# Optimization experiments

Measured on AMD Instinct MI355X. Metric: run time of the kernel, lower is better.

The kernel has to match this reference:

```python
import jax, jax.numpy as jnp
import numpy as np

B, T, E, H = 8, 2048, 1024, 1024
_LN_EPS = 1e-3  # keras LayerNormalization default epsilon


def _ln(x, g, b):
    mu = jnp.mean(x, axis=-1, keepdims=True)
    var = jnp.var(x, axis=-1, keepdims=True)
    return (x - mu) * jax.lax.rsqrt(var + _LN_EPS) * g + b


def _time_shift(x):
    # ZeroPadding1D((1,0)) applied to x[:, :-1]: shift right by one, zero at t=0
    return jnp.pad(x[:, :-1], ((0, 0), (1, 0), (0, 0)))


def _wkv(k, v, w, u):
    """RWKV-v4 wkv: numerically stabilized exponential-decay recurrence.
    k, v: (B, T, H); w = -exp(time_decay) (negative), u = time_first: (H,).
    wkv_t = (sum_{i<t} e^{(t-1-i)w + k_i} v_i + e^{u + k_t} v_t)
          / (sum_{i<t} e^{(t-1-i)w + k_i}     + e^{u + k_t})
    """
    Bk, Tk, Hk = k.shape

    def step(carry, kv_t):
        aa, bb, pp = carry  # running num/den with shared log-scale pp
        kt, vt = kv_t
        ww = u + kt
        q = jnp.maximum(pp, ww)
        e1 = jnp.exp(pp - q)
        e2 = jnp.exp(ww - q)
        out = (e1 * aa + e2 * vt) / (e1 * bb + e2)
        ww2 = pp + w
        q2 = jnp.maximum(ww2, kt)
        e1b = jnp.exp(ww2 - q2)
        e2b = jnp.exp(kt - q2)
        return (e1b * aa + e2b * vt, e1b * bb + e2b, q2), out

    init = (jnp.zeros((Bk, Hk), k.dtype),
            jnp.zeros((Bk, Hk), k.dtype),
            jnp.full((Bk, Hk), -1e38, k.dtype))
    kT = jnp.swapaxes(k, 0, 1)  # (T, B, H)
    vT = jnp.swapaxes(v, 0, 1)
    _, outs = jax.lax.scan(step, init, (kT, vT))
    return jnp.swapaxes(outs, 0, 1)


def setup_inputs() -> dict:
    key = jax.random.key(0)
    ks = jax.random.split(key, 20)

    def glorot(k, shape):
        lim = np.sqrt(6.0 / (shape[0] + shape[1]))
        return jax.random.uniform(k, shape, jnp.float32, -lim, lim)

    return {
        'inputs': jax.random.normal(ks[0], (B, T, E), jnp.float32),
        'ln1_g': jnp.ones((E,), jnp.float32),
        'ln1_b': jnp.zeros((E,), jnp.float32),
        'ln2_g': jnp.ones((E,), jnp.float32),
        'ln2_b': jnp.zeros((E,), jnp.float32),
        'tm_mix_k': jax.random.uniform(ks[1], (E,), jnp.float32, 0.0, 2.0 / E),
        'tm_mix_v': jax.random.uniform(ks[2], (E,), jnp.float32, 0.0, 2.0 / E),
        'tm_mix_r': jax.random.uniform(ks[3], (E,), jnp.float32, 0.0, (2.0 / E) ** 0.5),
        'tm_Wk': glorot(ks[4], (E, H)),
        'tm_Wv': glorot(ks[5], (E, H)),
        'tm_Wr': glorot(ks[6], (E, H)),
        'time_decay': jax.random.uniform(ks[7], (H,), jnp.float32, 0.0, 0.5),
        'time_first': jax.random.uniform(ks[8], (H,), jnp.float32, 0.0, 0.05),
        'Wo': glorot(ks[9], (H, E)),
        'cm_mix_k': jax.random.uniform(ks[10], (E,), jnp.float32, 0.0, 2.0 / E),
        'cm_mix_r': jax.random.uniform(ks[11], (E,), jnp.float32, 0.0, 2.0 / E),
        'cm_Wk': glorot(ks[12], (E, 4 * H)),
        'cm_Wv': glorot(ks[13], (4 * H, E)),
        'cm_Wr': glorot(ks[14], (E, E)),
    }


def reference(inputs, ln1_g, ln1_b, ln2_g, ln2_b,
              tm_mix_k, tm_mix_v, tm_mix_r, tm_Wk, tm_Wv, tm_Wr,
              time_decay, time_first, Wo,
              cm_mix_k, cm_mix_r, cm_Wk, cm_Wv, cm_Wr):
    x = inputs

    # ---- time mixing ----
    h = _ln(x, ln1_g, ln1_b)
    h1 = _time_shift(h)
    xk = h * tm_mix_k + h1 * (1.0 - tm_mix_k)
    xv = h * tm_mix_v + h1 * (1.0 - tm_mix_v)
    xr = h * tm_mix_r + h1 * (1.0 - tm_mix_r)
    k = xk @ tm_Wk
    v = xv @ tm_Wv
    r = xr @ tm_Wr
    wkv = _wkv(k, v, -jnp.exp(time_decay), time_first)
    x = x + (jax.nn.sigmoid(r) * wkv) @ Wo

    # ---- channel mixing ----
    h = _ln(x, ln2_g, ln2_b)
    h1 = _time_shift(h)
    xk = h * cm_mix_k + h1 * (1.0 - cm_mix_k)
    xr = h * cm_mix_r + h1 * (1.0 - cm_mix_r)
    kc = jnp.square(jax.nn.relu(xk @ cm_Wk))  # (B, T, 4H)
    rc = jax.nn.sigmoid(xr @ cm_Wr)
    x = x + rc * (kc @ cm_Wv)
    return x
```

## Files before the change

### kernel.cpp

```cpp
#include <hip/hip_runtime.h>
#include <stdint.h>
#include <stddef.h>

#define Bb 8
#define Tt 2048
#define Ee 1024
#define Hh 1024
#define ROWS (Bb * Tt)
#define CC 32
#define LL 64

typedef __attribute__((ext_vector_type(8))) _Float16 half8v;
typedef __attribute__((ext_vector_type(4))) _Float16 half4v;
typedef __attribute__((ext_vector_type(4))) float f32x4;

#define GL2LDS(gp, lp)                                                        \
  __builtin_amdgcn_global_load_lds(                                          \
      (const __attribute__((address_space(1))) void*)(gp),                   \
      (__attribute__((address_space(3))) void*)(lp), 16, 0, 0)

__global__ __launch_bounds__(256)
void wtrans_kernel(const float* __restrict__ W, _Float16* __restrict__ Wt,
                   const int K, const int N) {
  __shared__ float tle[64][65];
  const int ntn = N >> 6;
  const int tn = blockIdx.x % ntn;
  const int tk = blockIdx.x / ntn;
  const int tid = threadIdx.x;
  const int r = tid >> 4;
  const int c4 = (tid & 15) * 4;
#pragma unroll
  for (int i = 0; i < 4; i++) {
    const int row = r + i * 16;
    const float4 v = *reinterpret_cast<const float4*>(
        &W[(size_t)(tk * 64 + row) * N + tn * 64 + c4]);
    tle[row][c4] = v.x; tle[row][c4 + 1] = v.y;
    tle[row][c4 + 2] = v.z; tle[row][c4 + 3] = v.w;
  }
  __syncthreads();
#pragma unroll
  for (int j = 0; j < 2; j++) {
    const int ch = tid + j * 256;
    const int n = ch >> 3;
    const int k8 = (ch & 7) * 8;
    half8v o;
#pragma unroll
    for (int m = 0; m < 8; m++) o[m] = (_Float16)tle[k8 + m][n];
    *reinterpret_cast<half8v*>(&Wt[(size_t)(tn * 64 + n) * K + tk * 64 + k8]) = o;
  }
}

__global__ __launch_bounds__(256)
void ln_kernel(const float* __restrict__ x, const float* __restrict__ gw,
               const float* __restrict__ bw, _Float16* __restrict__ h) {
  const int row = blockIdx.x * 4 + (threadIdx.x >> 6);
  const int lane = threadIdx.x & 63;
  const float4* xr = reinterpret_cast<const float4*>(x + (size_t)row * Ee);
  float4 v[4];
  float s = 0.f, sq = 0.f;
#pragma unroll
  for (int i = 0; i < 4; i++) {
    v[i] = xr[lane + i * 64];
    s += v[i].x + v[i].y + v[i].z + v[i].w;
    sq += v[i].x * v[i].x + v[i].y * v[i].y + v[i].z * v[i].z + v[i].w * v[i].w;
  }
#pragma unroll
  for (int o = 32; o > 0; o >>= 1) {
    s += __shfl_xor(s, o);
    sq += __shfl_xor(sq, o);
  }
  const float mu = s * (1.f / Ee);
  const float var = sq * (1.f / Ee) - mu * mu;
  const float rs = rsqrtf(var + 1e-3f);
  const float4* gr = reinterpret_cast<const float4*>(gw);
  const float4* br = reinterpret_cast<const float4*>(bw);
#pragma unroll
  for (int i = 0; i < 4; i++) {
    const int c = lane + i * 64;
    const float4 g4 = gr[c], b4 = br[c];
    half4v o;
    o[0] = (_Float16)((v[i].x - mu) * rs * g4.x + b4.x);
    o[1] = (_Float16)((v[i].y - mu) * rs * g4.y + b4.y);
    o[2] = (_Float16)((v[i].z - mu) * rs * g4.z + b4.z);
    o[3] = (_Float16)((v[i].w - mu) * rs * g4.w + b4.w);
    *reinterpret_cast<half4v*>(&h[(size_t)row * Ee + (size_t)c * 4]) = o;
  }
}

template <bool HASV>
__global__ __launch_bounds__(256)
void mix_kernel(const _Float16* __restrict__ h, const float* __restrict__ mk,
                const float* __restrict__ mv, const float* __restrict__ mr,
                _Float16* __restrict__ xk, _Float16* __restrict__ xv,
                _Float16* __restrict__ xr) {
  const int gid = blockIdx.x * 256 + threadIdx.x;
  const int row = gid >> 8;
  const int c = gid & 255;
  const int t = row & (Tt - 1);
  const size_t o = (size_t)row * 1024 + (size_t)c * 4;
  const half4v hv4 = *reinterpret_cast<const half4v*>(&h[o]);
  float hx[4] = {(float)hv4[0], (float)hv4[1], (float)hv4[2], (float)hv4[3]};
  float h1[4] = {0.f, 0.f, 0.f, 0.f};
  if (t > 0) {
    const half4v p4 = *reinterpret_cast<const half4v*>(&h[o - 1024]);
    h1[0] = (float)p4[0]; h1[1] = (float)p4[1];
    h1[2] = (float)p4[2]; h1[3] = (float)p4[3];
  }
  const float4 k4 = reinterpret_cast<const float4*>(mk)[c];
  const float4 r4 = reinterpret_cast<const float4*>(mr)[c];
  const float km[4] = {k4.x, k4.y, k4.z, k4.w};
  const float rm[4] = {r4.x, r4.y, r4.z, r4.w};
  half4v ok, orr;
#pragma unroll
  for (int j = 0; j < 4; j++) {
    ok[j] = (_Float16)(hx[j] * km[j] + h1[j] * (1.f - km[j]));
    orr[j] = (_Float16)(hx[j] * rm[j] + h1[j] * (1.f - rm[j]));
  }
  *reinterpret_cast<half4v*>(&xk[o]) = ok;
  *reinterpret_cast<half4v*>(&xr[o]) = orr;
  if constexpr (HASV) {
    const float4 v4 = reinterpret_cast<const float4*>(mv)[c];
    const float vm[4] = {v4.x, v4.y, v4.z, v4.w};
    half4v ov;
#pragma unroll
    for (int j = 0; j < 4; j++)
      ov[j] = (_Float16)(hx[j] * vm[j] + h1[j] * (1.f - vm[j]));
    *reinterpret_cast<half4v*>(&xv[o]) = ov;
  }
}

__global__ __launch_bounds__(256)
void wkv_pass1(const _Float16* __restrict__ kb, const _Float16* __restrict__ vb,
               const float* __restrict__ decay,
               float* __restrict__ aal, float* __restrict__ bbl,
               float* __restrict__ ppl) {
  const int gid = blockIdx.x * 256 + threadIdx.x;
  const int h = gid & 1023;
  const int rest = gid >> 10;
  const int c = rest & (CC - 1);
  const int b = rest >> 5;
  const float w = -__expf(decay[h]);
  const size_t base = ((size_t)b * Tt + (size_t)c * LL) * Hh + h;
  float aa = 0.f, bb = 0.f, pp = -1e38f;
  for (int i0 = 0; i0 < LL; i0 += 8) {
    float kt[8], vt[8];
#pragma unroll
    for (int j = 0; j < 8; j++) {
      const size_t idx = base + (size_t)(i0 + j) * Hh;
      kt[j] = (float)kb[idx];
      vt[j] = (float)vb[idx];
    }
#pragma unroll
    for (int j = 0; j < 8; j++) {
      const float ww2 = pp + w;
      const float q2 = fmaxf(ww2, kt[j]);
      const float e1 = __expf(ww2 - q2);
      const float e2 = __expf(kt[j] - q2);
      aa = e1 * aa + e2 * vt[j];
      bb = e1 * bb + e2;
      pp = q2;
    }
  }
  const int sidx = (b * CC + c) * Hh + h;
  aal[sidx] = aa; bbl[sidx] = bb; ppl[sidx] = pp;
}

__global__ __launch_bounds__(256)
void wkv_pass2(const float* __restrict__ decay,
               const float* __restrict__ aal, const float* __restrict__ bbl,
               const float* __restrict__ ppl,
               float* __restrict__ aap, float* __restrict__ bbp,
               float* __restrict__ ppp) {
  const int gid = blockIdx.x * 256 + threadIdx.x;
  const int h = gid & 1023;
  const int b = gid >> 10;
  const float w = -__expf(decay[h]);
  const float Lw = (float)LL * w;
  float aa = 0.f, bb = 0.f, pp = -1e38f;
#pragma unroll
  for (int c = 0; c < CC; c++) {
    const int sidx = (b * CC + c) * Hh + h;
    aap[sidx] = aa; bbp[sidx] = bb; ppp[sidx] = pp;
    const float la = aal[sidx], lb = bbl[sidx], lp = ppl[sidx];
    const float sp = pp + Lw;
    const float q = fmaxf(sp, lp);
    const float e1 = __expf(sp - q);
    const float e2 = __expf(lp - q);
    aa = e1 * aa + e2 * la;
    bb = e1 * bb + e2 * lb;
    pp = q;
  }
}

__global__ __launch_bounds__(256)
void wkv_pass3(const _Float16* __restrict__ kb, const _Float16* __restrict__ vb,
               const _Float16* __restrict__ rb,
               const float* __restrict__ decay, const float* __restrict__ first,
               const float* __restrict__ aap, const float* __restrict__ bbp,
               const float* __restrict__ ppp, _Float16* __restrict__ ab) {
  const int gid = blockIdx.x * 256 + threadIdx.x;
  const int h = gid & 1023;
  const int rest = gid >> 10;
  const int c = rest & (CC - 1);
  const int b = rest >> 5;
  const float w = -__expf(decay[h]);
  const float u = first[h];
  const int sidx = (b * CC + c) * Hh + h;
  float aa = aap[sidx], bb = bbp[sidx], pp = ppp[sidx];
  const size_t base = ((size_t)b * Tt + (size_t)c * LL) * Hh + h;
  for (int i0 = 0; i0 < LL; i0 += 8) {
    float kt[8], vt[8], rr[8];
#pragma unroll
    for (int j = 0; j < 8; j++) {
      const size_t idx = base + (size_t)(i0 + j) * Hh;
      kt[j] = (float)kb[idx];
      vt[j] = (float)vb[idx];
      rr[j] = (float)rb[idx];
    }
#pragma unroll
    for (int j = 0; j < 8; j++) {
      const float ww = u + kt[j];
      const float q = fmaxf(pp, ww);
      const float e1 = __expf(pp - q);
      const float e2 = __expf(ww - q);
      const float out = (e1 * aa + e2 * vt[j]) / (e1 * bb + e2);
      const float sr = 1.f / (1.f + __expf(-rr[j]));
      ab[base + (size_t)(i0 + j) * Hh] = (_Float16)(sr * out);
      const float ww2 = pp + w;
      const float q2 = fmaxf(ww2, kt[j]);
      const float e1b = __expf(ww2 - q2);
      const float e2b = __expf(kt[j] - q2);
      aa = e1b * aa + e2b * vt[j];
      bb = e1b * bb + e2b;
      pp = q2;
    }
  }
}

template <int EPI>
__global__ __launch_bounds__(256)
void gemm97(const _Float16* __restrict__ A, const int ldA,
            const _Float16* __restrict__ Bt, const int ldB,
            const int N, const int K, const int nbx,
            float* __restrict__ outF, _Float16* __restrict__ outH,
            const float* __restrict__ res, const _Float16* __restrict__ scale) {
  alignas(16) __shared__ _Float16 As[128 * 64];
  alignas(16) __shared__ _Float16 Bs[128 * 64];
  const int tid = threadIdx.x;
  const int lane = tid & 63;
  const int w = tid >> 6;
  const int wm = w >> 1, wn = w & 1;
  const int r0 = lane & 15, kg = lane >> 4;
  const int cpx = gridDim.x >> 3;
  const int wg = ((int)blockIdx.x & 7) * cpx + ((int)blockIdx.x >> 3);
  const int bm = (wg / nbx) * 128;
  const int bn = (wg % nbx) * 128;
  const int NT = K >> 6;

  const int srow = lane >> 3;
  const int sslot = lane & 7;
  f32x4 acc[4][4];
#pragma unroll
  for (int i = 0; i < 4; i++)
#pragma unroll
    for (int j = 0; j < 4; j++) acc[i][j] = (f32x4){0.f, 0.f, 0.f, 0.f};

  for (int t = 0; t < NT; ++t) {
#pragma unroll
    for (int i = 0; i < 4; i++) {
      const int chunk = i * 4 + w;
      const int row = chunk * 8 + srow;
      const int gsl = sslot ^ (row & 7);
      GL2LDS(A + (size_t)(bm + row) * ldA + (size_t)t * 64 + gsl * 8,
             &As[chunk * 512]);
    }
#pragma unroll
    for (int i = 0; i < 4; i++) {
      const int chunk = i * 4 + w;
      const int row = chunk * 8 + srow;
      const int gsl = sslot ^ (row & 7);
      GL2LDS(Bt + (size_t)(bn + row) * ldB + (size_t)t * 64 + gsl * 8,
             &Bs[chunk * 512]);
    }
    __syncthreads();
    half8v af[4][2], bf[4][2];
#pragma unroll
    for (int m = 0; m < 4; m++)
#pragma unroll
      for (int kk = 0; kk < 2; kk++) {
        const int row = wm * 64 + m * 16 + r0;
        const int c = kk * 4 + kg;
        af[m][kk] = *reinterpret_cast<const half8v*>(
            &As[row * 64 + ((c ^ (row & 7)) << 3)]);
      }
#pragma unroll
    for (int n = 0; n < 4; n++)
#pragma unroll
      for (int kk = 0; kk < 2; kk++) {
        const int row = wn * 64 + n * 16 + r0;
        const int c = kk * 4 + kg;
        bf[n][kk] = *reinterpret_cast<const half8v*>(
            &Bs[row * 64 + ((c ^ (row & 7)) << 3)]);
      }
#pragma unroll
    for (int m = 0; m < 4; m++)
#pragma unroll
      for (int n = 0; n < 4; n++)
#pragma unroll
        for (int kk = 0; kk < 2; kk++)
          acc[m][n] = __builtin_amdgcn_mfma_f32_16x16x32_f16(
              af[m][kk], bf[n][kk], acc[m][n], 0, 0, 0);
    __syncthreads();
  }

#pragma unroll
  for (int m = 0; m < 4; m++) {
#pragma unroll
    for (int n = 0; n < 4; n++) {
#pragma unroll
      for (int i = 0; i < 4; i++) {
        const int row = bm + wm * 64 + m * 16 + kg * 4 + i;
        const int col = bn + wn * 64 + n * 16 + r0;
        const size_t idx = (size_t)row * N + col;
        const float val = acc[m][n][i];
        if constexpr (EPI == 0) {
          outH[idx] = (_Float16)val;
        } else if constexpr (EPI == 1) {
          const float tt = fmaxf(val, 0.f);
          outH[idx] = (_Float16)(tt * tt);
        } else if constexpr (EPI == 2) {
          outH[idx] = (_Float16)(1.f / (1.f + __expf(-val)));
        } else if constexpr (EPI == 3) {
          outF[idx] = res[idx] + val;
        } else {
          outF[idx] = outF[idx] + (float)scale[idx] * val;
        }
      }
    }
  }
}

extern "C" void kernel_launch(void* const* d_in, const int* in_sizes, int n_in,
                              void* d_out, int out_size, void* d_ws,
                              size_t ws_size, hipStream_t stream) {
  (void)in_sizes; (void)n_in; (void)out_size; (void)ws_size;
  const float* x_in      = (const float*)d_in[0];
  const float* ln1_g     = (const float*)d_in[1];
  const float* ln1_b     = (const float*)d_in[2];
  const float* ln2_g     = (const float*)d_in[3];
  const float* ln2_b     = (const float*)d_in[4];
  const float* tm_mix_k  = (const float*)d_in[5];
  const float* tm_mix_v  = (const float*)d_in[6];
  const float* tm_mix_r  = (const float*)d_in[7];
  const float* tm_Wk     = (const float*)d_in[8];
  const float* tm_Wv     = (const float*)d_in[9];
  const float* tm_Wr     = (const float*)d_in[10];
  const float* time_decay= (const float*)d_in[11];
  const float* time_first= (const float*)d_in[12];
  const float* Wo        = (const float*)d_in[13];
  const float* cm_mix_k  = (const float*)d_in[14];
  const float* cm_mix_r  = (const float*)d_in[15];
  const float* cm_Wk     = (const float*)d_in[16];
  const float* cm_Wv     = (const float*)d_in[17];
  const float* cm_Wr     = (const float*)d_in[18];
  float* out = (float*)d_out;
  char* ws = (char*)d_ws;
  const size_t MB = 1024ull * 1024ull;

  _Float16* WkT   = (_Float16*)(ws + 0 * MB);
  _Float16* WvT   = (_Float16*)(ws + 2 * MB);
  _Float16* WrT   = (_Float16*)(ws + 4 * MB);
  _Float16* WoT   = (_Float16*)(ws + 6 * MB);
  _Float16* cmWkT = (_Float16*)(ws + 8 * MB);
  _Float16* cmWvT = (_Float16*)(ws + 16 * MB);
  _Float16* cmWrT = (_Float16*)(ws + 24 * MB);
  float* aal = (float*)(ws + 0 * MB);
  float* bbl = (float*)(ws + 1 * MB);
  float* ppl = (float*)(ws + 2 * MB);
  float* aap = (float*)(ws + 3 * MB);
  float* bbp = (float*)(ws + 4 * MB);
  float* ppp = (float*)(ws + 5 * MB);
  _Float16* h16   = (_Float16*)(ws + 26 * MB);
  _Float16* xk    = (_Float16*)(ws + 58 * MB);
  _Float16* xv    = (_Float16*)(ws + 90 * MB);
  _Float16* xr    = (_Float16*)(ws + 122 * MB);
  _Float16* kb    = h16;
  _Float16* vb    = xk;
  _Float16* rb    = xv;
  _Float16* ab    = xr;
  _Float16* h2    = (_Float16*)(ws + 26 * MB);
  _Float16* xr2   = (_Float16*)(ws + 58 * MB);
  _Float16* xk2   = (_Float16*)(ws + 90 * MB);
  _Float16* rc    = (_Float16*)(ws + 122 * MB);
  _Float16* kc    = (_Float16*)(ws + 26 * MB);

  wtrans_kernel<<<dim3(256), 256, 0, stream>>>(tm_Wk, WkT, 1024, 1024);
  wtrans_kernel<<<dim3(256), 256, 0, stream>>>(tm_Wv, WvT, 1024, 1024);
  wtrans_kernel<<<dim3(256), 256, 0, stream>>>(tm_Wr, WrT, 1024, 1024);
  wtrans_kernel<<<dim3(256), 256, 0, stream>>>(Wo, WoT, 1024, 1024);
  wtrans_kernel<<<dim3(1024), 256, 0, stream>>>(cm_Wk, cmWkT, 1024, 4096);
  wtrans_kernel<<<dim3(1024), 256, 0, stream>>>(cm_Wv, cmWvT, 4096, 1024);
  wtrans_kernel<<<dim3(256), 256, 0, stream>>>(cm_Wr, cmWrT, 1024, 1024);

  ln_kernel<<<dim3(ROWS / 4), 256, 0, stream>>>(x_in, ln1_g, ln1_b, h16);
  mix_kernel<true><<<dim3(ROWS), 256, 0, stream>>>(h16, tm_mix_k, tm_mix_v,
                                                   tm_mix_r, xk, xv, xr);
  gemm97<0><<<dim3(128 * 8), 256, 0, stream>>>(xk, 1024, WkT, 1024, 1024, 1024,
                                               8, nullptr, kb, nullptr, nullptr);
  gemm97<0><<<dim3(128 * 8), 256, 0, stream>>>(xv, 1024, WvT, 1024, 1024, 1024,
                                               8, nullptr, vb, nullptr, nullptr);
  gemm97<0><<<dim3(128 * 8), 256, 0, stream>>>(xr, 1024, WrT, 1024, 1024, 1024,
                                               8, nullptr, rb, nullptr, nullptr);
  wkv_pass1<<<dim3(Bb * CC * Hh / 256), 256, 0, stream>>>(kb, vb, time_decay,
                                                          aal, bbl, ppl);
  wkv_pass2<<<dim3(Bb * Hh / 256), 256, 0, stream>>>(time_decay, aal, bbl, ppl,
                                                     aap, bbp, ppp);
  wkv_pass3<<<dim3(Bb * CC * Hh / 256), 256, 0, stream>>>(
      kb, vb, rb, time_decay, time_first, aap, bbp, ppp, ab);
  gemm97<3><<<dim3(128 * 8), 256, 0, stream>>>(ab, 1024, WoT, 1024, 1024, 1024,
                                               8, out, nullptr, x_in, nullptr);

  ln_kernel<<<dim3(ROWS / 4), 256, 0, stream>>>(out, ln2_g, ln2_b, h2);
  mix_kernel<false><<<dim3(ROWS), 256, 0, stream>>>(h2, cm_mix_k, nullptr,
                                                    cm_mix_r, xk2, nullptr, xr2);
  gemm97<2><<<dim3(128 * 8), 256, 0, stream>>>(xr2, 1024, cmWrT, 1024, 1024,
                                               1024, 8, nullptr, rc, nullptr,
                                               nullptr);
  for (int half = 0; half < 2; half++) {
    const _Float16* Bk = cmWkT + (size_t)half * 2048 * 1024;
    const _Float16* Bv = cmWvT + (size_t)half * 2048;
    gemm97<1><<<dim3(128 * 16), 256, 0, stream>>>(xk2, 1024, Bk, 1024, 2048,
                                                  1024, 16, nullptr, kc, nullptr,
                                                  nullptr);
    gemm97<4><<<dim3(128 * 8), 256, 0, stream>>>(kc, 2048, Bv, 4096, 1024,
                                                 2048, 8, out, nullptr, nullptr,
                                                 rc);
  }
}
```

Baseline: 864.0 us.

## Replace GEMM with 256x256-tile double-buffered kernel loading B directly to registers

The 128x128 GEMM with 256 threads becomes a 256x256-tile kernel with 512 threads (8 waves, 2x4). Only A is staged into double-buffered dynamic LDS; B fragments are loaded straight from global memory into registers, prefetched one K-step ahead. Explicit vmcnt waits, a single barrier per iteration and s_setprio around the MFMA block are meant to overlap loads with compute and cut LDS traffic and sync cost. The trade-offs are heavy register pressure from 128 accumulators plus two B fragment sets, uncoalesced direct B loads, and far fewer workgroups (256 for most GEMMs) to fill the GPU.

```diff
diff --git a/kernel.cpp b/kernel.cpp
--- a/kernel.cpp
+++ b/kernel.cpp
@@ -18,6 +18,10 @@
   __builtin_amdgcn_global_load_lds(                                          \
       (const __attribute__((address_space(1))) void*)(gp),                   \
       (__attribute__((address_space(3))) void*)(lp), 16, 0, 0)
+
+#define VMCNT(n) __builtin_amdgcn_s_waitcnt(0xF70 | (n))
+#define BAR __builtin_amdgcn_s_barrier()
+#define SCHED0 __builtin_amdgcn_sched_barrier(0)
 
 __global__ __launch_bounds__(256)
 void wtrans_kernel(const float* __restrict__ W, _Float16* __restrict__ Wt,
@@ -238,91 +242,104 @@
 }
 
 template <int EPI>
-__global__ __launch_bounds__(256)
-void gemm97(const _Float16* __restrict__ A, const int ldA,
+__global__ __launch_bounds__(512)
+void gemmBD(const _Float16* __restrict__ A, const int ldA,
             const _Float16* __restrict__ Bt, const int ldB,
             const int N, const int K, const int nbx,
             float* __restrict__ outF, _Float16* __restrict__ outH,
             const float* __restrict__ res, const _Float16* __restrict__ scale) {
-  alignas(16) __shared__ _Float16 As[128 * 64];
-  alignas(16) __shared__ _Float16 Bs[128 * 64];
+  extern __shared__ _Float16 sA[];
   const int tid = threadIdx.x;
   const int lane = tid & 63;
   const int w = tid >> 6;
-  const int wm = w >> 1, wn = w & 1;
+  const int wm = w >> 2, wn = w & 3;
   const int r0 = lane & 15, kg = lane >> 4;
   const int cpx = gridDim.x >> 3;
   const int wg = ((int)blockIdx.x & 7) * cpx + ((int)blockIdx.x >> 3);
-  const int bm = (wg / nbx) * 128;
-  const int bn = (wg % nbx) * 128;
+  const int bm = (wg / nbx) * 256;
+  const int bn = (wg % nbx) * 256;
   const int NT = K >> 6;
 
-  const int srow = lane >> 3;
-  const int sslot = lane & 7;
-  f32x4 acc[4][4];
-#pragma unroll
-  for (int i = 0; i < 4; i++)
+  f32x4 acc[8][4];
+#pragma unroll
+  for (int i = 0; i < 8; i++)
 #pragma unroll
     for (int j = 0; j < 4; j++) acc[i][j] = (f32x4){0.f, 0.f, 0.f, 0.f};
 
+  auto stageA = [&](int t, int p) {
+#pragma unroll
+    for (int i = 0; i < 4; i++) {
+      const int chunk = w * 4 + i;
+      const int row = chunk * 8 + (lane >> 3);
+      const int gs = (lane & 7) ^ (row & 7);
+      GL2LDS(A + (size_t)(bm + row) * ldA + (size_t)t * 64 + gs * 8,
+             sA + p * 16384 + chunk * 512);
+    }
+  };
+  auto loadB = [&](int t, half8v (&b)[4][2]) {
+#pragma unroll
+    for (int fc = 0; fc < 4; fc++)
+#pragma unroll
+      for (int kk = 0; kk < 2; kk++)
+        b[fc][kk] = *reinterpret_cast<const half8v*>(
+            Bt + (size_t)(bn + wn * 64 + fc * 16 + r0) * ldB +
+            (size_t)t * 64 + (size_t)(kk * 4 + kg) * 8);
+  };
+
+  half8v bC[4][2], bN[4][2];
+
+  stageA(0, 0);
+  VMCNT(0);
+  loadB(0, bC);
+  BAR;
+
   for (int t = 0; t < NT; ++t) {
-#pragma unroll
-    for (int i = 0; i < 4; i++) {
-      const int chunk = i * 4 + w;
-      const int row = chunk * 8 + srow;
-      const int gsl = sslot ^ (row & 7);
-      GL2LDS(A + (size_t)(bm + row) * ldA + (size_t)t * 64 + gsl * 8,
-             &As[chunk * 512]);
-    }
-#pragma unroll
-    for (int i = 0; i < 4; i++) {
-      const int chunk = i * 4 + w;
-      const int row = chunk * 8 + srow;
-      const int gsl = sslot ^ (row & 7);
-      GL2LDS(Bt + (size_t)(bn + row) * ldB + (size_t)t * 64 + gsl * 8,
-             &Bs[chunk * 512]);
-    }
-    __syncthreads();
-    half8v af[4][2], bf[4][2];
-#pragma unroll
-    for (int m = 0; m < 4; m++)
+    const int p = t & 1;
+    if (t + 1 < NT) stageA(t + 1, p ^ 1);
+    SCHED0;
+    half8v af[8][2];
+#pragma unroll
+    for (int fr = 0; fr < 8; fr++)
 #pragma unroll
       for (int kk = 0; kk < 2; kk++) {
-        const int row = wm * 64 + m * 16 + r0;
-        const int c = kk * 4 + kg;
-        af[m][kk] = *reinterpret_cast<const half8v*>(
-            &As[row * 64 + ((c ^ (row & 7)) << 3)]);
+        const int row = wm * 128 + fr * 16 + r0;
+        af[fr][kk] = *reinterpret_cast<const half8v*>(
+            sA + p * 16384 + row * 64 + (((kk * 4 + kg) ^ (row & 7)) << 3));
       }
-#pragma unroll
-    for (int n = 0; n < 4; n++)
-#pragma unroll
-      for (int kk = 0; kk < 2; kk++) {
-        const int row = wn * 64 + n * 16 + r0;
-        const int c = kk * 4 + kg;
-        bf[n][kk] = *reinterpret_cast<const half8v*>(
-            &Bs[row * 64 + ((c ^ (row & 7)) << 3)]);
-      }
-#pragma unroll
-    for (int m = 0; m < 4; m++)
-#pragma unroll
-      for (int n = 0; n < 4; n++)
+    __builtin_amdgcn_s_setprio(1);
+#pragma unroll
+    for (int fr = 0; fr < 8; fr++)
+#pragma unroll
+      for (int fc = 0; fc < 4; fc++)
 #pragma unroll
         for (int kk = 0; kk < 2; kk++)
-          acc[m][n] = __builtin_amdgcn_mfma_f32_16x16x32_f16(
-              af[m][kk], bf[n][kk], acc[m][n], 0, 0, 0);
-    __syncthreads();
-  }
-
-#pragma unroll
-  for (int m = 0; m < 4; m++) {
-#pragma unroll
-    for (int n = 0; n < 4; n++) {
+          acc[fr][fc] = __builtin_amdgcn_mfma_f32_16x16x32_f16(
+              af[fr][kk], bC[fc][kk], acc[fr][fc], 0, 0, 0);
+    __builtin_amdgcn_s_setprio(0);
+    SCHED0;
+    if (t + 1 < NT) {
+      loadB(t + 1, bN);
+      VMCNT(8);
+    } else {
+      VMCNT(0);
+    }
+    BAR;
+#pragma unroll
+    for (int fc = 0; fc < 4; fc++)
+#pragma unroll
+      for (int kk = 0; kk < 2; kk++) bC[fc][kk] = bN[fc][kk];
+  }
+
+#pragma unroll
+  for (int fr = 0; fr < 8; fr++) {
+#pragma unroll
+    for (int fc = 0; fc < 4; fc++) {
 #pragma unroll
       for (int i = 0; i < 4; i++) {
-        const int row = bm + wm * 64 + m * 16 + kg * 4 + i;
-        const int col = bn + wn * 64 + n * 16 + r0;
+        const int row = bm + wm * 128 + fr * 16 + (lane >> 4) * 4 + i;
+        const int col = bn + wn * 64 + fc * 16 + r0;
         const size_t idx = (size_t)row * N + col;
-        const float val = acc[m][n][i];
+        const float val = acc[fr][fc][i];
         if constexpr (EPI == 0) {
           outH[idx] = (_Float16)val;
         } else if constexpr (EPI == 1) {
@@ -394,6 +411,17 @@
   _Float16* rc    = (_Float16*)(ws + 122 * MB);
   _Float16* kc    = (_Float16*)(ws + 26 * MB);
 
+  const int SMEM = 65536;
+  static bool attr_done = false;
+  if (!attr_done) {
+    hipFuncSetAttribute((const void*)gemmBD<0>, hipFuncAttributeMaxDynamicSharedMemorySize, SMEM);
+    hipFuncSetAttribute((const void*)gemmBD<1>, hipFuncAttributeMaxDynamicSharedMemorySize, SMEM);
+    hipFuncSetAttribute((const void*)gemmBD<2>, hipFuncAttributeMaxDynamicSharedMemorySize, SMEM);
+    hipFuncSetAttribute((const void*)gemmBD<3>, hipFuncAttributeMaxDynamicSharedMemorySize, SMEM);
+    hipFuncSetAttribute((const void*)gemmBD<4>, hipFuncAttributeMaxDynamicSharedMemorySize, SMEM);
+    attr_done = true;
+  }
+
   wtrans_kernel<<<dim3(256), 256, 0, stream>>>(tm_Wk, WkT, 1024, 1024);
   wtrans_kernel<<<dim3(256), 256, 0, stream>>>(tm_Wv, WvT, 1024, 1024);
   wtrans_kernel<<<dim3(256), 256, 0, stream>>>(tm_Wr, WrT, 1024, 1024);
@@ -405,35 +433,39 @@
   ln_kernel<<<dim3(ROWS / 4), 256, 0, stream>>>(x_in, ln1_g, ln1_b, h16);
   mix_kernel<true><<<dim3(ROWS), 256, 0, stream>>>(h16, tm_mix_k, tm_mix_v,
                                                    tm_mix_r, xk, xv, xr);
-  gemm97<0><<<dim3(128 * 8), 256, 0, stream>>>(xk, 1024, WkT, 1024, 1024, 1024,
-                                               8, nullptr, kb, nullptr, nullptr);
-  gemm97<0><<<dim3(128 * 8), 256, 0, stream>>>(xv, 1024, WvT, 1024, 1024, 1024,
-                                               8, nullptr, vb, nullptr, nullptr);
-  gemm97<0><<<dim3(128 * 8), 256, 0, stream>>>(xr, 1024, WrT, 1024, 1024, 1024,
-                                               8, nullptr, rb, nullptr, nullptr);
+  gemmBD<0><<<dim3(64 * 4), 512, SMEM, stream>>>(xk, 1024, WkT, 1024, 1024,
+                                                 1024, 4, nullptr, kb, nullptr,
+                                                 nullptr);
+  gemmBD<0><<<dim3(64 * 4), 512, SMEM, stream>>>(xv, 1024, WvT, 1024, 1024,
+                                                 1024, 4, nullptr, vb, nullptr,
+                                                 nullptr);
+  gemmBD<0><<<dim3(64 * 4), 512, SMEM, stream>>>(xr, 1024, WrT, 1024, 1024,
+                                                 1024, 4, nullptr, rb, nullptr,
+                                                 nullptr);
   wkv_pass1<<<dim3(Bb * CC * Hh / 256), 256, 0, stream>>>(kb, vb, time_decay,
                                                           aal, bbl, ppl);
   wkv_pass2<<<dim3(Bb * Hh / 256), 256, 0, stream>>>(time_decay, aal, bbl, ppl,
                                                      aap, bbp, ppp);
   wkv_pass3<<<dim3(Bb * CC * Hh / 256), 256, 0, stream>>>(
       kb, vb, rb, time_decay, time_first, aap, bbp, ppp, ab);
-  gemm97<3><<<dim3(128 * 8), 256, 0, stream>>>(ab, 1024, WoT, 1024, 1024, 1024,
-                                               8, out, nullptr, x_in, nullptr);
+  gemmBD<3><<<dim3(64 * 4), 512, SMEM, stream>>>(ab, 1024, WoT, 1024, 1024,
+                                                 1024, 4, out, nullptr, x_in,
+                                                 nullptr);
 
   ln_kernel<<<dim3(ROWS / 4), 256, 0, stream>>>(out, ln2_g, ln2_b, h2);
   mix_kernel<false><<<dim3(ROWS), 256, 0, stream>>>(h2, cm_mix_k, nullptr,
                                                     cm_mix_r, xk2, nullptr, xr2);
-  gemm97<2><<<dim3(128 * 8), 256, 0, stream>>>(xr2, 1024, cmWrT, 1024, 1024,
-                                               1024, 8, nullptr, rc, nullptr,
-                                               nullptr);
+  gemmBD<2><<<dim3(64 * 4), 512, SMEM, stream>>>(xr2, 1024, cmWrT, 1024, 1024,
+                                                 1024, 4, nullptr, rc, nullptr,
+                                                 nullptr);
   for (int half = 0; half < 2; half++) {
     const _Float16* Bk = cmWkT + (size_t)half * 2048 * 1024;
     const _Float16* Bv = cmWvT + (size_t)half * 2048;
-    gemm97<1><<<dim3(128 * 16), 256, 0, stream>>>(xk2, 1024, Bk, 1024, 2048,
-                                                  1024, 16, nullptr, kc, nullptr,
-                                                  nullptr);
-    gemm97<4><<<dim3(128 * 8), 256, 0, stream>>>(kc, 2048, Bv, 4096, 1024,
-                                                 2048, 8, out, nullptr, nullptr,
-                                                 rc);
-  }
-}
+    gemmBD<1><<<dim3(64 * 8), 512, SMEM, stream>>>(xk2, 1024, Bk, 1024, 2048,
+                                                   1024, 8, nullptr, kc,
+                                                   nullptr, nullptr);
+    gemmBD<4><<<dim3(64 * 4), 512, SMEM, stream>>>(kc, 2048, Bv, 4096, 1024,
+                                                   2048, 4, out, nullptr,
+                                                   nullptr, rc);
+  }
+}
```

Result: slower. 901.1 us (+4.3%).
